# Kernel tuning notes

Hardware: AMD Instinct MI355X
Metric: run time of the kernel (lower is better)

The kernel has to match this reference:

```python
import jax, jax.numpy as jnp
import numpy as np

CONF = 0.3      # confidence threshold (NMS.conf)
IOU = 0.6       # IoU threshold (NMS.iou)
MAX_WH = 4096.0 # class-offset trick for per-class NMS
K = 2048        # max candidates entering NMS (yolov5-style cap)
MAX_DET = 300   # max detections kept per image (fixed output size)


def setup_inputs() -> dict:
    key = jax.random.key(0)
    kxy, kwh, kobj, kcls = jax.random.split(key, 4)
    B, N, NC = 8, 25200, 80
    # realistic raw predictions: xywh in pixel units for a 640x640 image
    xy = jax.random.uniform(kxy, (B, N, 2), minval=0.0, maxval=640.0)
    wh = jax.random.uniform(kwh, (B, N, 2), minval=2.0, maxval=160.0)
    obj = jax.random.uniform(kobj, (B, N, 1))
    cls = jax.random.uniform(kcls, (B, N, NC))
    x = jnp.concatenate([xy, wh, obj, cls], axis=-1)  # [B, N, 5+NC]
    return {"x": x}


def _xywh2xyxy(b):
    xy, half = b[..., :2], b[..., 2:4] * 0.5
    return jnp.concatenate([xy - half, xy + half], axis=-1)


def _pairwise_iou(boxes):  # boxes: [K, 4] xyxy -> [K, K]
    lt = jnp.maximum(boxes[:, None, :2], boxes[None, :, :2])
    rb = jnp.minimum(boxes[:, None, 2:], boxes[None, :, 2:])
    inter = jnp.clip(rb - lt, 0.0).prod(-1)
    area = (boxes[:, 2] - boxes[:, 0]) * (boxes[:, 3] - boxes[:, 1])
    return inter / (area[:, None] + area[None, :] - inter + 1e-9)


def _nms_single(pred):  # pred: [N, 5+NC]
    obj = pred[:, 4]
    cls_conf = pred[:, 5:] * obj[:, None]          # conf = obj * cls prob
    conf = cls_conf.max(-1)
    cls_id = jnp.argmax(cls_conf, -1)
    valid = (obj > CONF) & (conf > CONF)           # candidate + final threshold
    boxes = _xywh2xyxy(pred[:, :4])
    scores = jnp.where(valid, conf, -1.0)
    top_s, idx = jax.lax.top_k(scores, K)          # cap candidates, sorted desc
    boxes_k = boxes[idx]
    cls_k = cls_id[idx]
    valid_k = top_s > 0.0
    # offset boxes by class so NMS is per-class
    shifted = boxes_k + cls_k[:, None].astype(boxes_k.dtype) * MAX_WH
    iou = _pairwise_iou(shifted)                   # [K, K]
    order = jnp.arange(K)

    def body(keep, i):  # greedy suppression in score order
        active = keep[i] & valid_k[i]
        sup = (iou[i] > IOU) & (order > i)
        keep = jnp.where(active, keep & ~sup, keep)
        return keep, None

    keep, _ = jax.lax.scan(body, jnp.ones((K,), bool), order)
    keep = keep & valid_k
    final_s = jnp.where(keep, top_s, -1.0)
    det_s, det_i = jax.lax.top_k(final_s, MAX_DET)
    dets = jnp.concatenate(
        [boxes_k[det_i], top_s[det_i][:, None],
         cls_k[det_i][:, None].astype(boxes_k.dtype)], axis=-1)  # [MAX_DET, 6]
    return dets, det_s > 0.0


def reference(x):
    # returns (dets [B, MAX_DET, 6] = xyxy,conf,cls ; valid mask [B, MAX_DET])
    return jax.vmap(_nms_single)(x)
```

## Files before the change

### kernel.cpp

```cpp
#include <hip/hip_runtime.h>

#define B 8
#define N 25200
#define ROW 85
#define NC 80
#define K 2048
#define MAXDET 300
#define NBUCKET 4096
#define CAND_CAP 4096
#define NCHUNK 32
#define STILE 64
#define CTR_STRIDE 64

__global__ void __launch_bounds__(256)
nms_score_kernel(const float* __restrict__ x,
                 float* __restrict__ scores,
                 int* __restrict__ cls_id,
                 float4* __restrict__ boxes4,
                 unsigned* __restrict__ ready,
                 unsigned* __restrict__ done_ctr,
                 unsigned long long* __restrict__ keepbits) {
    int b = blockIdx.y;
    int i0 = blockIdx.x * STILE;
    if (blockIdx.x == 0) {
        if (threadIdx.x == 0) {
            ready[b * CTR_STRIDE] = 0u;
            done_ctr[b * CTR_STRIDE] = 0u;
        }
        if (threadIdx.x < NCHUNK) keepbits[b * NCHUNK + threadIdx.x] = 0ULL;
    }
    int rows = N - i0; if (rows > STILE) rows = STILE;
    __shared__ float lx[STILE * ROW];
    {
        const float4* s4 = (const float4*)(x + ((size_t)b * N + i0) * ROW);
        float4* d4 = (float4*)lx;
        int nv = rows * ROW / 4;
        for (int k = threadIdx.x; k < nv; k += 256) d4[k] = s4[k];
    }
    __syncthreads();
    int g = threadIdx.x >> 2;
    int q = threadIdx.x & 3;
    if (g >= rows) return;
    const float* p = lx + g * ROW;
    float obj = p[4];
    float best = -1e30f;
    int bc = 127;
    if (obj > 0.3f) {
        #pragma unroll
        for (int k = 0; k < 20; ++k) {
            int c = q + 4 * k;
            float v = __fmul_rn(p[5 + c], obj);
            if (v > best) { best = v; bc = c; }
        }
    }
    #pragma unroll
    for (int m = 1; m < 4; m <<= 1) {
        float ov = __shfl_xor(best, m, 64);
        int   oc = __shfl_xor(bc, m, 64);
        if (ov > best || (ov == best && oc < bc)) { best = ov; bc = oc; }
    }
    if (q == 0) {
        int i = i0 + g;
        float score = (obj > 0.3f && best > 0.3f) ? best : -1.0f;
        scores[b * N + i] = score;
        cls_id[b * N + i] = (bc == 127) ? 0 : bc;
        float cx = p[0], cy = p[1], w = p[2], h = p[3];
        float hx = __fmul_rn(w, 0.5f);
        float hy = __fmul_rn(h, 0.5f);
        boxes4[b * N + i] = make_float4(__fsub_rn(cx, hx), __fsub_rn(cy, hy),
                                        __fadd_rn(cx, hx), __fadd_rn(cy, hy));
    }
}

__global__ void __launch_bounds__(1024, 1)
nms_tail_kernel(const float* __restrict__ scores,
                const float4* __restrict__ boxes4,
                const int* __restrict__ cls_id,
                unsigned long long* __restrict__ gkeys,
                unsigned long long* __restrict__ keepbits,
                unsigned* __restrict__ ready,
                unsigned* __restrict__ done_ctr,
                float* __restrict__ out) {
    __shared__ union {
        struct {
            unsigned loff[NBUCKET];
            unsigned lcnt16[NBUCKET / 2];
            unsigned long long lk[CAND_CAP];
        } s;
        struct {
            unsigned long long keys[K];
            unsigned long long lcm[NC * NCHUNK];
            unsigned long long kept[NCHUNK];
            unsigned kcpref[NCHUNK];
            int total;
            int oflag;
        } c;
    } U;
    __shared__ unsigned wsum[16];

    int bid = blockIdx.x;
    int t = threadIdx.x;
    int ln = t & 63, wv = t >> 6;
    unsigned long long below = (ln == 0) ? 0ULL : (~0ULL >> (64 - ln));

    if (bid < B) {
        int b = bid;
        constexpr int NITER = (N + 1023) / 1024;

        {
            uint4 z = {0u, 0u, 0u, 0u};
            uint4* d1 = (uint4*)U.s.loff;
            for (int k = t; k < (NBUCKET + NBUCKET / 2) / 4; k += 1024) d1[k] = z;
        }
        for (int k = t; k < CAND_CAP; k += 1024) U.s.lk[k] = 0ULL;
        __syncthreads();

        float sreg[NITER];
        #pragma unroll
        for (int r = 0; r < NITER; ++r) {
            int i = t + r * 1024;
            float s = (i < N) ? scores[b * N + i] : -1.0f;
            sreg[r] = s;
            if (s > 0.0f) {
                int q = (int)(__fmul_rn(s, 4096.0f));
                if (q > NBUCKET - 1) q = NBUCKET - 1;
                atomicAdd(&U.s.loff[q], 1u);
            }
        }
        __syncthreads();

        unsigned v[4];
        unsigned A4 = (unsigned)(NBUCKET / 4 - 1 - t);
        {
            uint4 u0 = ((uint4*)U.s.loff)[A4];
            v[0] = u0.w; v[1] = u0.z; v[2] = u0.y; v[3] = u0.x;
        }
        unsigned S = v[0] + v[1] + v[2] + v[3];
        unsigned pref = S;
        #pragma unroll
        for (int o = 1; o < 64; o <<= 1) { unsigned u = __shfl_up(pref, o, 64); if (ln >= o) pref += u; }
        if (ln == 63) wsum[wv] = pref;
        __syncthreads();
        unsigned wbase = 0;
        for (int w = 0; w < wv; ++w) wbase += wsum[w];
        unsigned running = wbase + pref - S;
        {
            unsigned o[4];
            #pragma unroll
            for (int k = 0; k < 4; ++k) { o[3 - k] = running; running += v[k]; }
            ((uint4*)U.s.loff)[A4] = make_uint4(o[0], o[1], o[2], o[3]);
        }
        __syncthreads();

        #pragma unroll
        for (int r = 0; r < NITER; ++r) {
            float s = sreg[r];
            if (s > 0.0f) {
                int i = t + r * 1024;
                int q = (int)(__fmul_rn(s, 4096.0f));
                if (q > NBUCKET - 1) q = NBUCKET - 1;
                unsigned start = U.s.loff[q];
                if (start < CAND_CAP) {
                    unsigned sh = (q & 1) * 16;
                    unsigned old = atomicAdd(&U.s.lcnt16[q >> 1], 1u << sh);
                    unsigned rank = (old >> sh) & 0xFFFFu;
                    unsigned pos = start + rank;
                    if (pos < CAND_CAP) {
                        unsigned long long key =
                            ((unsigned long long)__float_as_uint(s) << 32) | (unsigned)(~i);
                        U.s.lk[pos] = key;
                    }
                }
            }
        }
        __syncthreads();

        for (int q = t; q < NBUCKET; q += 1024) {
            unsigned start = U.s.loff[q];
            if (start < CAND_CAP) {
                unsigned c = (U.s.lcnt16[q >> 1] >> ((q & 1) * 16)) & 0xFFFFu;
                unsigned m = c;
                if (m > CAND_CAP - start) m = CAND_CAP - start;
                if (m >= 2) {
                    for (unsigned a = start + 1; a < start + m; ++a) {
                        unsigned long long kv = U.s.lk[a];
                        unsigned p2 = a;
                        while (p2 > start && U.s.lk[p2 - 1] < kv) { U.s.lk[p2] = U.s.lk[p2 - 1]; --p2; }
                        U.s.lk[p2] = kv;
                    }
                }
            }
        }
        __syncthreads();

        for (int r = t; r < K; r += 1024)
            gkeys[(size_t)b * K + r] = U.s.lk[r];
        __syncthreads();
        if (t == 0) {
            __threadfence();
            atomicExch(&ready[b * CTR_STRIDE], 1u);
        }
        return;
    }

    int gid = bid - B;
    int b = gid / 5;
    int grp = gid % 5;
    int c = grp * 16 + wv;

    if (t == 0) {
        U.c.oflag = 0;
        while (atomicOr(&ready[b * CTR_STRIDE], 0u) == 0u)
            __builtin_amdgcn_s_sleep(8);
        __threadfence();
    }
    __syncthreads();

    for (int r = t; r < K; r += 1024) U.c.keys[r] = gkeys[(size_t)b * K + r];
    for (int k = t; k < NC * NCHUNK; k += 1024) U.c.lcm[k] = 0ULL;
    __syncthreads();

    for (int r = t; r < K; r += 1024) {
        unsigned long long key = U.c.keys[r];
        if (key != 0ULL) {
            int idx = (int)(~(unsigned)key);
            int cc = cls_id[b * N + idx];
            atomicOr(&U.c.lcm[cc * NCHUNK + (r >> 6)], 1ULL << (r & 63));
        }
    }
    __syncthreads();

    int n = 0, r = -1, ch_i = -1, myk = -1;
    unsigned long long mych = 0ULL;
    for (int ch = 0; ch < NCHUNK; ++ch) {
        unsigned long long m = U.c.lcm[c * NCHUNK + ch];
        int cnt = __popcll(m);
        if (myk < 0 && ln < n + cnt) { mych = m; myk = ln - n; ch_i = ch; }
        n += cnt;
    }
    if (myk >= 0) {
        unsigned long long mm = mych;
        for (int z = 0; z < myk; ++z) mm &= mm - 1;
        r = ch_i * 64 + (int)__builtin_ctzll(mm);
    }

    float shf = __fmul_rn((float)c, 4096.0f);

    if (n > 0 && n <= 64) {
        float x1 = 0.f, y1 = 0.f, x2 = 0.f, y2 = 0.f, ar = 0.f;
        if (ln < n) {
            unsigned long long key = U.c.keys[r];
            int idx = (int)(~(unsigned)key);
            float4 bb = boxes4[(size_t)b * N + idx];
            x1 = __fadd_rn(bb.x, shf); y1 = __fadd_rn(bb.y, shf);
            x2 = __fadd_rn(bb.z, shf); y2 = __fadd_rn(bb.w, shf);
            ar = __fmul_rn(__fsub_rn(x2, x1), __fsub_rn(y2, y1));
        }
        unsigned long long keepw = (n == 64) ? ~0ULL : ((1ULL << n) - 1ULL);
        for (int i = 0; i < n; ++i) {
            if (!((keepw >> i) & 1ULL)) continue;
            float bx1 = __shfl(x1, i, 64), by1 = __shfl(y1, i, 64);
            float bx2 = __shfl(x2, i, 64), by2 = __shfl(y2, i, 64);
            float ba  = __shfl(ar, i, 64);
            bool cond = false;
            if (ln > i && ln < n) {
                float lx = fmaxf(bx1, x1), ly = fmaxf(by1, y1);
                float rx = fminf(bx2, x2), ry = fminf(by2, y2);
                float w = fmaxf(__fsub_rn(rx, lx), 0.0f);
                float h = fmaxf(__fsub_rn(ry, ly), 0.0f);
                float inter = __fmul_rn(w, h);
                float denom = __fadd_rn(__fsub_rn(__fadd_rn(ba, ar), inter), 1e-9f);
                cond = __fdiv_rn(inter, denom) > 0.6f;
            }
            keepw &= ~__ballot(cond);
        }
        if (ln < n && ((keepw >> ln) & 1ULL))
            atomicOr(&keepbits[b * NCHUNK + (r >> 6)], 1ULL << (r & 63));
    } else if (n > 64) {
        unsigned long long membw = (ln < NCHUNK) ? U.c.lcm[c * NCHUNK + ln] : 0ULL;
        unsigned long long keepw2 = membw;
        for (int i = 0; i < K; ++i) {
            int ch = i >> 6;
            unsigned long long mw = __shfl(membw, ch, 64);
            unsigned long long kw = __shfl(keepw2, ch, 64);
            unsigned long long bi = 1ULL << (i & 63);
            if (!(mw & kw & bi)) continue;
            unsigned long long keyi = U.c.keys[i];
            int idxi = (int)(~(unsigned)keyi);
            float4 bi4 = boxes4[(size_t)b * N + idxi];
            float bx1 = __fadd_rn(bi4.x, shf), by1 = __fadd_rn(bi4.y, shf);
            float bx2 = __fadd_rn(bi4.z, shf), by2 = __fadd_rn(bi4.w, shf);
            float ba = __fmul_rn(__fsub_rn(bx2, bx1), __fsub_rn(by2, by1));
            for (int c2 = ch; c2 < NCHUNK; ++c2) {
                int j = c2 * 64 + ln;
                unsigned long long mw2 = __shfl(membw, c2, 64);
                bool cond = false;
                if (j > i && ((mw2 >> ln) & 1ULL)) {
                    unsigned long long keyj = U.c.keys[j];
                    int idxj = (int)(~(unsigned)keyj);
                    float4 bj4 = boxes4[(size_t)b * N + idxj];
                    float x1 = __fadd_rn(bj4.x, shf), y1 = __fadd_rn(bj4.y, shf);
                    float x2 = __fadd_rn(bj4.z, shf), y2 = __fadd_rn(bj4.w, shf);
                    float arj = __fmul_rn(__fsub_rn(x2, x1), __fsub_rn(y2, y1));
                    float lx = fmaxf(bx1, x1), ly = fmaxf(by1, y1);
                    float rx = fminf(bx2, x2), ry = fminf(by2, y2);
                    float w = fmaxf(__fsub_rn(rx, lx), 0.0f);
                    float h = fmaxf(__fsub_rn(ry, ly), 0.0f);
                    float inter = __fmul_rn(w, h);
                    float denom = __fadd_rn(__fsub_rn(__fadd_rn(ba, arj), inter), 1e-9f);
                    cond = __fdiv_rn(inter, denom) > 0.6f;
                }
                unsigned long long sup = __ballot(cond);
                if (ln == c2) keepw2 &= ~sup;
            }
        }
        if (ln < NCHUNK && (keepw2 & membw))
            atomicOr(&keepbits[b * NCHUNK + ln], keepw2 & membw);
    }

    __threadfence();
    unsigned old = 0;
    if (ln == 0) old = atomicAdd(&done_ctr[b * CTR_STRIDE], 1u);
    old = (unsigned)__shfl((int)old, 0, 64);
    if (old == NC - 1) {
        __threadfence();
        unsigned long long kwv = 0ULL;
        if (ln < NCHUNK) kwv = atomicOr(&keepbits[b * NCHUNK + ln], 0ULL);
        unsigned pc = (unsigned)__popcll(kwv);
        unsigned incl = pc;
        #pragma unroll
        for (int o = 1; o < 32; o <<= 1) { unsigned u = __shfl_up(incl, o, 64); if (ln >= o) incl += u; }
        if (ln < NCHUNK) {
            U.c.kept[ln] = kwv;
            U.c.kcpref[ln] = incl - pc;
        }
        if (ln == 31) U.c.total = (int)incl;
        if (ln == 0)  U.c.oflag = 1;
    }
    __syncthreads();

    if (U.c.oflag) {
        int total = U.c.total;
        float* dets  = out + (size_t)b * MAXDET * 6;
        float* flags = out + (size_t)B * MAXDET * 6 + (size_t)b * MAXDET;
        #pragma unroll
        for (int h = 0; h < 2; ++h) {
            int ch = wv * 2 + h;
            int i = ch * 64 + ln;
            unsigned long long m = U.c.kept[ch];
            bool k = ((m >> ln) & 1ULL) != 0ULL;
            int kp = (int)U.c.kcpref[ch];
            int np = ch * 64 - kp;
            int slot = k ? (kp + (int)__popcll(m & below))
                         : (total + np + (int)__popcll((~m) & below));
            if (slot < MAXDET) {
                unsigned long long key = U.c.keys[i];
                float s, ox1, oy1, ox2, oy2; int oc;
                if (key == 0ULL) {
                    s = -1.0f; ox1 = oy1 = ox2 = oy2 = 0.0f; oc = 0;
                } else {
                    s = __uint_as_float((unsigned)(key >> 32));
                    int idx = (int)(~(unsigned)key);
                    float4 bb = boxes4[(size_t)b * N + idx];
                    ox1 = bb.x; oy1 = bb.y; ox2 = bb.z; oy2 = bb.w;
                    oc = cls_id[b * N + idx];
                }
                dets[slot * 6 + 0] = ox1;
                dets[slot * 6 + 1] = oy1;
                dets[slot * 6 + 2] = ox2;
                dets[slot * 6 + 3] = oy2;
                dets[slot * 6 + 4] = s;
                dets[slot * 6 + 5] = (float)oc;
                flags[slot] = k ? 1.0f : 0.0f;
            }
        }
    }
}

extern "C" void kernel_launch(void* const* d_in, const int* in_sizes, int n_in,
                              void* d_out, int out_size, void* d_ws, size_t ws_size,
                              hipStream_t stream) {
    const float* x = (const float*)d_in[0];
    float* out = (float*)d_out;

    char* ws = (char*)d_ws;
    size_t off = 0;
    auto alloc = [&](size_t bytes) -> void* {
        void* p = ws + off;
        off += bytes;
        off = (off + 255) & ~(size_t)255;
        return p;
    };

    float*    scores = (float*)    alloc((size_t)B * N * 4);
    int*      cls_id = (int*)      alloc((size_t)B * N * 4);
    float4*   boxes4 = (float4*)   alloc((size_t)B * N * 16);
    unsigned long long* gkeys    = (unsigned long long*) alloc((size_t)B * K * 8);
    unsigned long long* keepbits = (unsigned long long*) alloc((size_t)B * NCHUNK * 8);
    unsigned* ready    = (unsigned*) alloc((size_t)B * CTR_STRIDE * 4);
    unsigned* done_ctr = (unsigned*) alloc((size_t)B * CTR_STRIDE * 4);
    (void)ws_size;

    nms_score_kernel<<<dim3((N + STILE - 1) / STILE, B), 256, 0, stream>>>(
        x, scores, cls_id, boxes4, ready, done_ctr, keepbits);
    nms_tail_kernel<<<B + 5 * B, 1024, 0, stream>>>(
        scores, boxes4, cls_id, gkeys, keepbits, ready, done_ctr, out);
}
```

Baseline: 139.6 us.

## Have each NMS group block redo the top-K selection instead of waiting on producer blocks

Removes the dedicated per-image top-K blocks, the global key buffer and the ready-flag spin-wait. Each of the five class-group blocks per image now builds its own histogram, bucket sort and candidate list in shared memory and uses the keys directly. This drops a global round trip and the inter-block handshake, which also removes the risk of spinning while producer blocks are not yet scheduled. The cost is that the selection work is repeated five times per image, adding score reads and shared-memory sorting work per block.

```diff
diff --git a/kernel.cpp b/kernel.cpp
--- a/kernel.cpp
+++ b/kernel.cpp
@@ -17,16 +17,12 @@
                  float* __restrict__ scores,
                  int* __restrict__ cls_id,
                  float4* __restrict__ boxes4,
-                 unsigned* __restrict__ ready,
                  unsigned* __restrict__ done_ctr,
                  unsigned long long* __restrict__ keepbits) {
     int b = blockIdx.y;
     int i0 = blockIdx.x * STILE;
     if (blockIdx.x == 0) {
-        if (threadIdx.x == 0) {
-            ready[b * CTR_STRIDE] = 0u;
-            done_ctr[b * CTR_STRIDE] = 0u;
-        }
+        if (threadIdx.x == 0) done_ctr[b * CTR_STRIDE] = 0u;
         if (threadIdx.x < NCHUNK) keepbits[b * NCHUNK + threadIdx.x] = 0ULL;
     }
     int rows = N - i0; if (rows > STILE) rows = STILE;
@@ -76,9 +72,7 @@
 nms_tail_kernel(const float* __restrict__ scores,
                 const float4* __restrict__ boxes4,
                 const int* __restrict__ cls_id,
-                unsigned long long* __restrict__ gkeys,
                 unsigned long long* __restrict__ keepbits,
-                unsigned* __restrict__ ready,
                 unsigned* __restrict__ done_ctr,
                 float* __restrict__ out) {
     __shared__ union {
@@ -103,32 +97,34 @@
     int ln = t & 63, wv = t >> 6;
     unsigned long long below = (ln == 0) ? 0ULL : (~0ULL >> (64 - ln));
 
-    if (bid < B) {
-        int b = bid;
-        constexpr int NITER = (N + 1023) / 1024;
-
-        {
-            uint4 z = {0u, 0u, 0u, 0u};
-            uint4* d1 = (uint4*)U.s.loff;
-            for (int k = t; k < (NBUCKET + NBUCKET / 2) / 4; k += 1024) d1[k] = z;
-        }
-        for (int k = t; k < CAND_CAP; k += 1024) U.s.lk[k] = 0ULL;
-        __syncthreads();
-
-        float sreg[NITER];
-        #pragma unroll
-        for (int r = 0; r < NITER; ++r) {
-            int i = t + r * 1024;
-            float s = (i < N) ? scores[b * N + i] : -1.0f;
-            sreg[r] = s;
-            if (s > 0.0f) {
-                int q = (int)(__fmul_rn(s, 4096.0f));
-                if (q > NBUCKET - 1) q = NBUCKET - 1;
-                atomicAdd(&U.s.loff[q], 1u);
-            }
-        }
-        __syncthreads();
-
+    int b = bid / 5;
+    int grp = bid % 5;
+    int c = grp * 16 + wv;
+    constexpr int NITER = (N + 1023) / 1024;
+
+    {
+        uint4 z = {0u, 0u, 0u, 0u};
+        uint4* d1 = (uint4*)U.s.loff;
+        for (int k = t; k < (NBUCKET + NBUCKET / 2) / 4; k += 1024) d1[k] = z;
+    }
+    for (int k = t; k < CAND_CAP; k += 1024) U.s.lk[k] = 0ULL;
+    __syncthreads();
+
+    float sreg[NITER];
+    #pragma unroll
+    for (int r = 0; r < NITER; ++r) {
+        int i = t + r * 1024;
+        float s = (i < N) ? scores[b * N + i] : -1.0f;
+        sreg[r] = s;
+        if (s > 0.0f) {
+            int q = (int)(__fmul_rn(s, 4096.0f));
+            if (q > NBUCKET - 1) q = NBUCKET - 1;
+            atomicAdd(&U.s.loff[q], 1u);
+        }
+    }
+    __syncthreads();
+
+    {
         unsigned v[4];
         unsigned A4 = (unsigned)(NBUCKET / 4 - 1 - t);
         {
@@ -144,80 +140,58 @@
         unsigned wbase = 0;
         for (int w = 0; w < wv; ++w) wbase += wsum[w];
         unsigned running = wbase + pref - S;
-        {
-            unsigned o[4];
-            #pragma unroll
-            for (int k = 0; k < 4; ++k) { o[3 - k] = running; running += v[k]; }
-            ((uint4*)U.s.loff)[A4] = make_uint4(o[0], o[1], o[2], o[3]);
-        }
-        __syncthreads();
-
-        #pragma unroll
-        for (int r = 0; r < NITER; ++r) {
-            float s = sreg[r];
-            if (s > 0.0f) {
-                int i = t + r * 1024;
-                int q = (int)(__fmul_rn(s, 4096.0f));
-                if (q > NBUCKET - 1) q = NBUCKET - 1;
-                unsigned start = U.s.loff[q];
-                if (start < CAND_CAP) {
-                    unsigned sh = (q & 1) * 16;
-                    unsigned old = atomicAdd(&U.s.lcnt16[q >> 1], 1u << sh);
-                    unsigned rank = (old >> sh) & 0xFFFFu;
-                    unsigned pos = start + rank;
-                    if (pos < CAND_CAP) {
-                        unsigned long long key =
-                            ((unsigned long long)__float_as_uint(s) << 32) | (unsigned)(~i);
-                        U.s.lk[pos] = key;
-                    }
-                }
-            }
-        }
-        __syncthreads();
-
-        for (int q = t; q < NBUCKET; q += 1024) {
+        unsigned o[4];
+        #pragma unroll
+        for (int k = 0; k < 4; ++k) { o[3 - k] = running; running += v[k]; }
+        ((uint4*)U.s.loff)[A4] = make_uint4(o[0], o[1], o[2], o[3]);
+    }
+    __syncthreads();
+
+    #pragma unroll
+    for (int r = 0; r < NITER; ++r) {
+        float s = sreg[r];
+        if (s > 0.0f) {
+            int i = t + r * 1024;
+            int q = (int)(__fmul_rn(s, 4096.0f));
+            if (q > NBUCKET - 1) q = NBUCKET - 1;
             unsigned start = U.s.loff[q];
             if (start < CAND_CAP) {
-                unsigned c = (U.s.lcnt16[q >> 1] >> ((q & 1) * 16)) & 0xFFFFu;
-                unsigned m = c;
-                if (m > CAND_CAP - start) m = CAND_CAP - start;
-                if (m >= 2) {
-                    for (unsigned a = start + 1; a < start + m; ++a) {
-                        unsigned long long kv = U.s.lk[a];
-                        unsigned p2 = a;
-                        while (p2 > start && U.s.lk[p2 - 1] < kv) { U.s.lk[p2] = U.s.lk[p2 - 1]; --p2; }
-                        U.s.lk[p2] = kv;
-                    }
+                unsigned sh = (q & 1) * 16;
+                unsigned old = atomicAdd(&U.s.lcnt16[q >> 1], 1u << sh);
+                unsigned rank = (old >> sh) & 0xFFFFu;
+                unsigned pos = start + rank;
+                if (pos < CAND_CAP) {
+                    unsigned long long key =
+                        ((unsigned long long)__float_as_uint(s) << 32) | (unsigned)(~i);
+                    U.s.lk[pos] = key;
                 }
             }
         }
-        __syncthreads();
-
-        for (int r = t; r < K; r += 1024)
-            gkeys[(size_t)b * K + r] = U.s.lk[r];
-        __syncthreads();
-        if (t == 0) {
-            __threadfence();
-            atomicExch(&ready[b * CTR_STRIDE], 1u);
-        }
-        return;
-    }
-
-    int gid = bid - B;
-    int b = gid / 5;
-    int grp = gid % 5;
-    int c = grp * 16 + wv;
-
-    if (t == 0) {
-        U.c.oflag = 0;
-        while (atomicOr(&ready[b * CTR_STRIDE], 0u) == 0u)
-            __builtin_amdgcn_s_sleep(8);
-        __threadfence();
-    }
-    __syncthreads();
-
-    for (int r = t; r < K; r += 1024) U.c.keys[r] = gkeys[(size_t)b * K + r];
+    }
+    __syncthreads();
+
+    for (int q = t; q < NBUCKET; q += 1024) {
+        unsigned start = U.s.loff[q];
+        if (start < CAND_CAP) {
+            unsigned cc = (U.s.lcnt16[q >> 1] >> ((q & 1) * 16)) & 0xFFFFu;
+            unsigned m = cc;
+            if (m > CAND_CAP - start) m = CAND_CAP - start;
+            if (m >= 2) {
+                for (unsigned a = start + 1; a < start + m; ++a) {
+                    unsigned long long kv = U.s.lk[a];
+                    unsigned p2 = a;
+                    while (p2 > start && U.s.lk[p2 - 1] < kv) { U.s.lk[p2] = U.s.lk[p2 - 1]; --p2; }
+                    U.s.lk[p2] = kv;
+                }
+            }
+        }
+    }
+    __syncthreads();
+
+    for (int r = t; r < K; r += 1024) U.c.keys[r] = U.s.lk[r];
+    __syncthreads();
     for (int k = t; k < NC * NCHUNK; k += 1024) U.c.lcm[k] = 0ULL;
+    if (t == 0) U.c.oflag = 0;
     __syncthreads();
 
     for (int r = t; r < K; r += 1024) {
@@ -395,14 +369,12 @@
     float*    scores = (float*)    alloc((size_t)B * N * 4);
     int*      cls_id = (int*)      alloc((size_t)B * N * 4);
     float4*   boxes4 = (float4*)   alloc((size_t)B * N * 16);
-    unsigned long long* gkeys    = (unsigned long long*) alloc((size_t)B * K * 8);
     unsigned long long* keepbits = (unsigned long long*) alloc((size_t)B * NCHUNK * 8);
-    unsigned* ready    = (unsigned*) alloc((size_t)B * CTR_STRIDE * 4);
     unsigned* done_ctr = (unsigned*) alloc((size_t)B * CTR_STRIDE * 4);
     (void)ws_size;
 
     nms_score_kernel<<<dim3((N + STILE - 1) / STILE, B), 256, 0, stream>>>(
-        x, scores, cls_id, boxes4, ready, done_ctr, keepbits);
-    nms_tail_kernel<<<B + 5 * B, 1024, 0, stream>>>(
-        scores, boxes4, cls_id, gkeys, keepbits, ready, done_ctr, out);
+        x, scores, cls_id, boxes4, done_ctr, keepbits);
+    nms_tail_kernel<<<5 * B, 1024, 0, stream>>>(
+        scores, boxes4, cls_id, keepbits, done_ctr, out);
 }
```

Result: faster. 136.3 us (-2.4%).
